# Performance work log

Hardware: AMD Instinct MI355X
Metric: run time of the kernel (lower is better)

The kernel has to match this reference:

```python
import jax, jax.numpy as jnp
import numpy as np

D_MODEL = 1024
N_HEADS = 16
D_K = D_MODEL // N_HEADS
NEG_INF = -1e30


def setup_inputs() -> dict:
    key = jax.random.key(0)
    ks = jax.random.split(key, 12)
    B, S = 4, 2048
    scale = 1.0 / np.sqrt(D_MODEL)
    inp = {
        "query": jax.random.normal(ks[0], (B, S, D_MODEL), jnp.float32),
        "key": jax.random.normal(ks[1], (B, S, D_MODEL), jnp.float32),
        "value": jax.random.normal(ks[2], (B, S, D_MODEL), jnp.float32),
        "mask": jax.random.randint(ks[3], (B, S, S), 0, 2, jnp.int32),
        "w_q": jax.random.normal(ks[4], (D_MODEL, D_MODEL), jnp.float32) * scale,
        "b_q": jnp.zeros((D_MODEL,), jnp.float32),
        "w_k": jax.random.normal(ks[5], (D_MODEL, D_MODEL), jnp.float32) * scale,
        "b_k": jnp.zeros((D_MODEL,), jnp.float32),
        "w_v": jax.random.normal(ks[6], (D_MODEL, D_MODEL), jnp.float32) * scale,
        "b_v": jnp.zeros((D_MODEL,), jnp.float32),
        "w_o": jax.random.normal(ks[7], (D_MODEL, D_MODEL), jnp.float32) * scale,
        "b_o": jnp.zeros((D_MODEL,), jnp.float32),
    }
    return inp


def reference(query, key, value, mask, w_q, b_q, w_k, b_k, w_v, b_v, w_o, b_o):
    B, Sq, _ = query.shape
    Sk = key.shape[1]
    # Linear projections (torch nn.Linear: x @ W.T + b), split into heads
    Q = (query @ w_q.T + b_q).reshape(B, Sq, N_HEADS, D_K).transpose(0, 2, 1, 3)
    K = (key @ w_k.T + b_k).reshape(B, Sk, N_HEADS, D_K).transpose(0, 2, 1, 3)
    V = (value @ w_v.T + b_v).reshape(B, Sk, N_HEADS, D_K).transpose(0, 2, 1, 3)
    # scores: (B, H, Sq, Sk)
    scores = jnp.einsum('bhqd,bhkd->bhqk', Q, K) / jnp.sqrt(jnp.float32(D_K))
    scores = jnp.where(mask[:, None, :, :] == 0, NEG_INF, scores)
    attn = jax.nn.softmax(scores, axis=-1)  # dropout p=0 -> identity (eval)
    context = jnp.einsum('bhqk,bhkd->bhqd', attn, V)
    context = context.transpose(0, 2, 1, 3).reshape(B, Sq, D_MODEL)
    return context @ w_o.T + b_o
```

## Files before the change

### kernel.cpp

```cpp
#include <hip/hip_runtime.h>
#include <hip/hip_bf16.h>
#include <stdint.h>

#define DM 1024
#define NHEADS 16
#define DK 64
#define BB 4
#define SS 2048

typedef unsigned short u16;
typedef __bf16 bf16x8 __attribute__((ext_vector_type(8)));
typedef __bf16 bf16x4 __attribute__((ext_vector_type(4)));
typedef float f32x4 __attribute__((ext_vector_type(4)));

#if __has_builtin(__builtin_amdgcn_exp2f)
#define EXP2(x) __builtin_amdgcn_exp2f(x)
#else
#define EXP2(x) exp2f(x)
#endif

static __device__ __forceinline__ u16 f2bf(float f) {
    union { float f; uint32_t u; } v; v.f = f;
    uint32_t r = v.u + 0x7fffu + ((v.u >> 16) & 1u);
    return (u16)(r >> 16);
}

static __device__ __forceinline__ f32x4 mfma16(bf16x8 a, bf16x8 b, f32x4 c) {
    return __builtin_amdgcn_mfma_f32_16x16x32_bf16(a, b, c, 0, 0, 0);
}

static __device__ __forceinline__ void gload16(const u16* g, u16* l) {
    __builtin_amdgcn_global_load_lds((const __attribute__((address_space(1))) void*)g,
                                     (__attribute__((address_space(3))) void*)l, 16, 0, 0);
}

__global__ void k_cvtw(const float* __restrict__ wq, const float* __restrict__ wk,
                       const float* __restrict__ wv, const float* __restrict__ wo,
                       u16* __restrict__ out) {
    int t = blockIdx.x * blockDim.x + threadIdx.x;
    int which = t >> 18;
    int off = (t & 0x3FFFF) << 2;
    const float* src = (which == 0) ? wq : (which == 1) ? wk : (which == 2) ? wv : wo;
    float4 v = *(const float4*)(src + off);
    ushort4 o;
    o.x = f2bf(v.x); o.y = f2bf(v.y); o.z = f2bf(v.z); o.w = f2bf(v.w);
    *(ushort4*)(out + ((size_t)which << 20) + off) = o;
}

__global__ void k_cvtx(const float* __restrict__ q, const float* __restrict__ k,
                       const float* __restrict__ v, u16* __restrict__ out) {
    int bid = blockIdx.x;
    int which = bid >> 12;
    const float* src = (which == 0) ? q : (which == 1) ? k : v;
    size_t base = (((size_t)(bid & 4095)) * 256 + threadIdx.x) * 8;
    float4 v0 = *(const float4*)(src + base);
    float4 v1 = *(const float4*)(src + base + 4);
    union { u16 s[8]; uint4 u; } p;
    p.s[0]=f2bf(v0.x); p.s[1]=f2bf(v0.y); p.s[2]=f2bf(v0.z); p.s[3]=f2bf(v0.w);
    p.s[4]=f2bf(v1.x); p.s[5]=f2bf(v1.y); p.s[6]=f2bf(v1.z); p.s[7]=f2bf(v1.w);
    *(uint4*)(out + ((size_t)which << 23) + base) = p.u;
}

__global__ void k_packmask(const int* __restrict__ mask, uint32_t* __restrict__ bits) {
    int gid = blockIdx.x * blockDim.x + threadIdx.x;
    int lane = gid & 63;
    int wv = gid >> 6;
    int nw = (gridDim.x * blockDim.x) >> 6;
    const long totalInts = (long)BB * SS * SS;
    for (long base = (long)wv * 64; base < totalInts; base += (long)nw * 64) {
        int m = mask[base + lane];
        unsigned long long bal = __ballot(m != 0);
        if (lane == 0)  bits[(base >> 5)]     = (uint32_t)bal;
        if (lane == 32) bits[(base >> 5) + 1] = (uint32_t)(bal >> 32);
    }
}

template<int MODE>
__global__ __launch_bounds__(256) void k_proj(const u16* __restrict__ X, const u16* __restrict__ W,
                                              const float* __restrict__ bias, void* __restrict__ Yv,
                                              float alpha) {
    __shared__ u16 Ab[128 * 32];
    __shared__ u16 Bb[128 * 32];
    const int tid = threadIdx.x;
    const int lane = tid & 63, wv = tid >> 6;
    const int wr = wv >> 1, wc = wv & 1;
    const int lrow = lane & 15, lgrp = lane >> 4;
    const int m0 = (blockIdx.x >> 3) * 128;
    const int n0 = (blockIdx.x & 7) * 128;
    const int trow = tid >> 2;
    const int tk = (tid & 3) * 8;

    f32x4 acc[4][4] = {};

    for (int kk = 0; kk < DM; kk += 32) {
#pragma unroll
        for (int i = 0; i < 2; ++i) {
            gload16(X + (size_t)(m0 + i * 64 + trow) * DM + kk + tk, &Ab[(i * 256 + tid) * 8]);
            gload16(W + (size_t)(n0 + i * 64 + trow) * DM + kk + tk, &Bb[(i * 256 + tid) * 8]);
        }
        __syncthreads();
        bf16x8 af[4], bfr[4];
#pragma unroll
        for (int i = 0; i < 4; ++i)
            af[i] = *(const bf16x8*)&Ab[(wr * 64 + i * 16 + lrow) * 32 + lgrp * 8];
#pragma unroll
        for (int j = 0; j < 4; ++j)
            bfr[j] = *(const bf16x8*)&Bb[(wc * 64 + j * 16 + lrow) * 32 + lgrp * 8];
#pragma unroll
        for (int i = 0; i < 4; ++i)
#pragma unroll
            for (int j = 0; j < 4; ++j)
                acc[i][j] = mfma16(af[i], bfr[j], acc[i][j]);
        __syncthreads();
    }

#pragma unroll
    for (int j = 0; j < 4; ++j) {
        int n = n0 + wc * 64 + j * 16 + lrow;
        float bv = bias[n];
        int h = n >> 6, d = n & 63;
#pragma unroll
        for (int i = 0; i < 4; ++i) {
            int mbase = m0 + wr * 64 + i * 16 + (lgrp << 2);
            if (MODE == 0) {
                u16* Y = (u16*)Yv;
#pragma unroll
                for (int r = 0; r < 4; ++r) {
                    int m = mbase + r;
                    int b = m >> 11, s = m & 2047;
                    Y[(((size_t)(b * NHEADS + h) * SS) + s) * DK + d] = f2bf((acc[i][j][r] + bv) * alpha);
                }
            } else if (MODE == 1) {
                int b = mbase >> 11, s = mbase & 2047;
                ushort4 o;
                o.x = f2bf(acc[i][j][0] + bv);
                o.y = f2bf(acc[i][j][1] + bv);
                o.z = f2bf(acc[i][j][2] + bv);
                o.w = f2bf(acc[i][j][3] + bv);
                *(ushort4*)&((u16*)Yv)[(((size_t)(b * NHEADS + h) * DK) + d) * SS + s] = o;
            } else {
                float* Y = (float*)Yv;
#pragma unroll
                for (int r = 0; r < 4; ++r)
                    Y[(size_t)(mbase + r) * DM + n] = acc[i][j][r] + bv;
            }
        }
    }
}

#define NT (SS / 64)
__global__ __launch_bounds__(256, 2) void k_attn(const u16* __restrict__ Q, const u16* __restrict__ K,
                                                 const u16* __restrict__ VT, const uint32_t* __restrict__ mbits,
                                                 u16* __restrict__ ctx) {
    __shared__ u16 Kt[2][64 * 64];
    __shared__ u16 Vt[2][64 * 64];
    __shared__ u16 Pl[4][2][16][72];
    const int tid = threadIdx.x;
    const int lane = tid & 63, w = tid >> 6;
    const int lrow = lane & 15, lgrp = lane >> 4;
    const int bid = blockIdx.x;
    const int x = bid & 7, rr_ = bid >> 3;
    const int h = (x & 3) + 4 * (rr_ & 3);
    const int qt = ((x >> 2) & 1) + 2 * ((rr_ >> 2) & 3);
    const int b = rr_ >> 4;
    const int bh = b * NHEADS + h;
    const int qbase = qt * 256 + w * 64;

    const u16* Qh = Q + (size_t)bh * SS * DK;
    const u16* Kh = K + (size_t)bh * SS * DK;
    const u16* Vh = VT + (size_t)bh * DK * SS;

    bf16x8 qf[4][2];
#pragma unroll
    for (int s = 0; s < 4; ++s) {
        const u16* p = Qh + (size_t)(qbase + 16 * s + lrow) * DK + lgrp * 8;
        qf[s][0] = *(const bf16x8*)(p);
        qf[s][1] = *(const bf16x8*)(p + 32);
    }

    const uint64_t* mrow[4];
#pragma unroll
    for (int s = 0; s < 4; ++s)
        mrow[s] = (const uint64_t*)mbits + ((size_t)(b * SS + qbase + 16 * s + lrow)) * (SS / 64);

    union { uint4 u; bf16x8 v; } onesu;
    onesu.u = make_uint4(0x3F803F80u, 0x3F803F80u, 0x3F803F80u, 0x3F803F80u);
    const bf16x8 ones = onesu.v;

    const int swzA = (lgrp * 8) ^ ((lrow & 7) * 8);
    const int swzB = (32 + lgrp * 8) ^ ((lrow & 7) * 8);

    f32x4 acc[4][4] = {};
    f32x4 asum[4] = {};

#pragma unroll
    for (int i = 0; i < 2; ++i) {
        int li = i * 256 + tid;
        int row = li >> 3;
        int src = ((li & 7) * 8) ^ ((row & 7) * 8);
        gload16(Kh + (size_t)(row)*DK + src, &Kt[0][li * 8]);
        gload16(Vh + (size_t)(row)*SS + src, &Vt[0][li * 8]);
    }
    __syncthreads();

    int cur = 0;
    for (int kt = 0; kt < NT; ++kt) {
        if (kt + 1 < NT) {
#pragma unroll
            for (int i = 0; i < 2; ++i) {
                int li = i * 256 + tid;
                int row = li >> 3;
                int src = ((li & 7) * 8) ^ ((row & 7) * 8);
                gload16(Kh + (size_t)((kt + 1) * 64 + row) * DK + src, &Kt[cur ^ 1][li * 8]);
                gload16(Vh + (size_t)(row)*SS + (kt + 1) * 64 + src, &Vt[cur ^ 1][li * 8]);
            }
        }
        uint64_t wm4[4];
#pragma unroll
        for (int s = 0; s < 4; ++s) wm4[s] = mrow[s][kt];

        const u16* Kc = Kt[cur];
        const u16* Vc = Vt[cur];
        bf16x8 pf[4][2];
#pragma unroll
        for (int sg = 0; sg < 2; ++sg) {
            f32x4 st[2][4] = {};
#pragma unroll
            for (int t = 0; t < 4; ++t) {
                bf16x8 ka = *(const bf16x8*)&Kc[(16 * t + lrow) * 64 + swzA];
                bf16x8 kb = *(const bf16x8*)&Kc[(16 * t + lrow) * 64 + swzB];
                st[0][t] = mfma16(ka, qf[2 * sg + 0][0], st[0][t]);
                st[0][t] = mfma16(kb, qf[2 * sg + 0][1], st[0][t]);
                st[1][t] = mfma16(ka, qf[2 * sg + 1][0], st[1][t]);
                st[1][t] = mfma16(kb, qf[2 * sg + 1][1], st[1][t]);
            }
#pragma unroll
            for (int s2 = 0; s2 < 2; ++s2) {
                const int s = 2 * sg + s2;
                const uint64_t wm = wm4[s];
#pragma unroll
                for (int t = 0; t < 4; ++t) {
                    uint32_t wt = (uint32_t)(wm >> (16 * t + 4 * lgrp));
                    bf16x4 pk;
#pragma unroll
                    for (int r = 0; r < 4; ++r) {
                        float p = EXP2(st[s2][t][r]);
                        p = ((wt >> r) & 1u) ? p : 0.0f;
                        pk[r] = (__bf16)p;
                    }
                    *(bf16x4*)&Pl[w][s2][lrow][16 * t + 4 * lgrp] = pk;
                }
            }
#pragma unroll
            for (int s2 = 0; s2 < 2; ++s2) {
                const int s = 2 * sg + s2;
                pf[s][0] = *(const bf16x8*)&Pl[w][s2][lrow][lgrp * 8];
                pf[s][1] = *(const bf16x8*)&Pl[w][s2][lrow][32 + lgrp * 8];
                asum[s] = mfma16(pf[s][0], ones, asum[s]);
                asum[s] = mfma16(pf[s][1], ones, asum[s]);
            }
        }
#pragma unroll
        for (int dt = 0; dt < 4; ++dt) {
            bf16x8 vf0 = *(const bf16x8*)&Vc[(16 * dt + lrow) * 64 + swzA];
            bf16x8 vf1 = *(const bf16x8*)&Vc[(16 * dt + lrow) * 64 + swzB];
#pragma unroll
            for (int s = 0; s < 4; ++s) {
                acc[s][dt] = mfma16(pf[s][0], vf0, acc[s][dt]);
                acc[s][dt] = mfma16(pf[s][1], vf1, acc[s][dt]);
            }
        }
        __syncthreads();
        cur ^= 1;
    }

#pragma unroll
    for (int s = 0; s < 4; ++s)
#pragma unroll
        for (int r = 0; r < 4; ++r) {
            float li = 1.0f / asum[s][r];
            int q = qbase + 16 * s + 4 * lgrp + r;
#pragma unroll
            for (int dt = 0; dt < 4; ++dt)
                ctx[((size_t)b * SS + q) * DM + h * 64 + dt * 16 + lrow] = f2bf(acc[s][dt][r] * li);
        }
}

extern "C" void kernel_launch(void* const* d_in, const int* in_sizes, int n_in,
                              void* d_out, int out_size, void* d_ws, size_t ws_size,
                              hipStream_t stream) {
    const float* query = (const float*)d_in[0];
    const float* key   = (const float*)d_in[1];
    const float* value = (const float*)d_in[2];
    const int*   mask  = (const int*)d_in[3];
    const float* w_q   = (const float*)d_in[4];
    const float* b_q   = (const float*)d_in[5];
    const float* w_k   = (const float*)d_in[6];
    const float* b_k   = (const float*)d_in[7];
    const float* w_v   = (const float*)d_in[8];
    const float* b_v   = (const float*)d_in[9];
    const float* w_o   = (const float*)d_in[10];
    const float* b_o   = (const float*)d_in[11];
    float* out = (float*)d_out;

    char* ws = (char*)d_ws;
    u16*      Wb = (u16*)(ws);
    uint32_t* mb = (uint32_t*)(ws + (8u  << 20));
    u16*      Xq = (u16*)(ws + (16u << 20));
    u16*      Xk = (u16*)(ws + (32u << 20));
    u16*      Xv = (u16*)(ws + (48u << 20));
    u16*      Qw = (u16*)(ws + (64u << 20));
    u16*      Kw = (u16*)(ws + (80u << 20));
    u16*      Vw = (u16*)(ws + (96u << 20));
    u16*      Cw = (u16*)(ws + (112u << 20));

    const float qscale = 0.125f * 1.4426950408889634f;

    k_cvtw<<<dim3(4096), dim3(256), 0, stream>>>(w_q, w_k, w_v, w_o, Wb);
    k_cvtx<<<dim3(12288), dim3(256), 0, stream>>>(query, key, value, Xq);
    k_packmask<<<dim3(2048), dim3(256), 0, stream>>>(mask, mb);
    k_proj<0><<<dim3(512), dim3(256), 0, stream>>>(Xq, Wb,              b_q, Qw, qscale);
    k_proj<0><<<dim3(512), dim3(256), 0, stream>>>(Xk, Wb + (1u << 20), b_k, Kw, 1.0f);
    k_proj<1><<<dim3(512), dim3(256), 0, stream>>>(Xv, Wb + (2u << 20), b_v, Vw, 1.0f);
    k_attn<<<dim3(512), dim3(256), 0, stream>>>(Qw, Kw, Vw, mb, Cw);
    k_proj<2><<<dim3(512), dim3(256), 0, stream>>>(Cw, Wb + (3u << 20), b_o, out, 1.0f);
}
```

Baseline: 287.9 us.

## Merge preprocessing kernels and widen attention blocks to 8 waves of 32 rows

```diff
diff --git a/kernel.cpp b/kernel.cpp
--- a/kernel.cpp
+++ b/kernel.cpp
@@ -34,44 +34,49 @@
                                      (__attribute__((address_space(3))) void*)l, 16, 0, 0);
 }
 
-__global__ void k_cvtw(const float* __restrict__ wq, const float* __restrict__ wk,
-                       const float* __restrict__ wv, const float* __restrict__ wo,
-                       u16* __restrict__ out) {
-    int t = blockIdx.x * blockDim.x + threadIdx.x;
-    int which = t >> 18;
-    int off = (t & 0x3FFFF) << 2;
-    const float* src = (which == 0) ? wq : (which == 1) ? wk : (which == 2) ? wv : wo;
-    float4 v = *(const float4*)(src + off);
-    ushort4 o;
-    o.x = f2bf(v.x); o.y = f2bf(v.y); o.z = f2bf(v.z); o.w = f2bf(v.w);
-    *(ushort4*)(out + ((size_t)which << 20) + off) = o;
-}
-
-__global__ void k_cvtx(const float* __restrict__ q, const float* __restrict__ k,
-                       const float* __restrict__ v, u16* __restrict__ out) {
-    int bid = blockIdx.x;
-    int which = bid >> 12;
-    const float* src = (which == 0) ? q : (which == 1) ? k : v;
-    size_t base = (((size_t)(bid & 4095)) * 256 + threadIdx.x) * 8;
-    float4 v0 = *(const float4*)(src + base);
-    float4 v1 = *(const float4*)(src + base + 4);
-    union { u16 s[8]; uint4 u; } p;
-    p.s[0]=f2bf(v0.x); p.s[1]=f2bf(v0.y); p.s[2]=f2bf(v0.z); p.s[3]=f2bf(v0.w);
-    p.s[4]=f2bf(v1.x); p.s[5]=f2bf(v1.y); p.s[6]=f2bf(v1.z); p.s[7]=f2bf(v1.w);
-    *(uint4*)(out + ((size_t)which << 23) + base) = p.u;
-}
-
-__global__ void k_packmask(const int* __restrict__ mask, uint32_t* __restrict__ bits) {
-    int gid = blockIdx.x * blockDim.x + threadIdx.x;
-    int lane = gid & 63;
-    int wv = gid >> 6;
-    int nw = (gridDim.x * blockDim.x) >> 6;
-    const long totalInts = (long)BB * SS * SS;
-    for (long base = (long)wv * 64; base < totalInts; base += (long)nw * 64) {
-        int m = mask[base + lane];
-        unsigned long long bal = __ballot(m != 0);
-        if (lane == 0)  bits[(base >> 5)]     = (uint32_t)bal;
-        if (lane == 32) bits[(base >> 5) + 1] = (uint32_t)(bal >> 32);
+#define PREP_W 4096
+#define PREP_X 12288
+#define PREP_M 2048
+__global__ __launch_bounds__(256) void k_prep(const float* __restrict__ wq, const float* __restrict__ wk,
+                                              const float* __restrict__ wv, const float* __restrict__ wo,
+                                              u16* __restrict__ wout,
+                                              const float* __restrict__ xq, const float* __restrict__ xk,
+                                              const float* __restrict__ xv, u16* __restrict__ xout,
+                                              const int* __restrict__ mask, uint32_t* __restrict__ bits) {
+    const int bid = blockIdx.x, tid = threadIdx.x;
+    if (bid < PREP_W) {
+        int t = bid * 256 + tid;
+        int which = t >> 18;
+        int off = (t & 0x3FFFF) << 2;
+        const float* src = (which == 0) ? wq : (which == 1) ? wk : (which == 2) ? wv : wo;
+        float4 v = *(const float4*)(src + off);
+        ushort4 o;
+        o.x = f2bf(v.x); o.y = f2bf(v.y); o.z = f2bf(v.z); o.w = f2bf(v.w);
+        *(ushort4*)(wout + ((size_t)which << 20) + off) = o;
+    } else if (bid < PREP_W + PREP_X) {
+        int lb = bid - PREP_W;
+        int which = lb >> 12;
+        const float* src = (which == 0) ? xq : (which == 1) ? xk : xv;
+        size_t base = (((size_t)(lb & 4095)) * 256 + tid) * 8;
+        float4 v0 = *(const float4*)(src + base);
+        float4 v1 = *(const float4*)(src + base + 4);
+        union { u16 s[8]; uint4 u; } p;
+        p.s[0]=f2bf(v0.x); p.s[1]=f2bf(v0.y); p.s[2]=f2bf(v0.z); p.s[3]=f2bf(v0.w);
+        p.s[4]=f2bf(v1.x); p.s[5]=f2bf(v1.y); p.s[6]=f2bf(v1.z); p.s[7]=f2bf(v1.w);
+        *(uint4*)(xout + ((size_t)which << 23) + base) = p.u;
+    } else {
+        int lb = bid - PREP_W - PREP_X;
+        int gid = lb * 256 + tid;
+        int lane = gid & 63;
+        int wv_ = gid >> 6;
+        const int nw = (PREP_M * 256) >> 6;
+        const long totalInts = (long)BB * SS * SS;
+        for (long base = (long)wv_ * 64; base < totalInts; base += (long)nw * 64) {
+            int m = mask[base + lane];
+            unsigned long long bal = __ballot(m != 0);
+            if (lane == 0)  bits[(base >> 5)]     = (uint32_t)bal;
+            if (lane == 32) bits[(base >> 5) + 1] = (uint32_t)(bal >> 32);
+        }
     }
 }
 
@@ -149,38 +154,36 @@
 }
 
 #define NT (SS / 64)
-__global__ __launch_bounds__(256, 2) void k_attn(const u16* __restrict__ Q, const u16* __restrict__ K,
+__global__ __launch_bounds__(512, 4) void k_attn(const u16* __restrict__ Q, const u16* __restrict__ K,
                                                  const u16* __restrict__ VT, const uint32_t* __restrict__ mbits,
                                                  u16* __restrict__ ctx) {
     __shared__ u16 Kt[2][64 * 64];
     __shared__ u16 Vt[2][64 * 64];
-    __shared__ u16 Pl[4][2][16][72];
+    __shared__ u16 Pl[8][2][16][72];
     const int tid = threadIdx.x;
     const int lane = tid & 63, w = tid >> 6;
     const int lrow = lane & 15, lgrp = lane >> 4;
     const int bid = blockIdx.x;
-    const int x = bid & 7, rr_ = bid >> 3;
-    const int h = (x & 3) + 4 * (rr_ & 3);
-    const int qt = ((x >> 2) & 1) + 2 * ((rr_ >> 2) & 3);
-    const int b = rr_ >> 4;
-    const int bh = b * NHEADS + h;
-    const int qbase = qt * 256 + w * 64;
+    const int bh = bid & 63;
+    const int qt = bid >> 6;
+    const int b = bh >> 4, h = bh & 15;
+    const int qbase = qt * 256 + w * 32;
 
     const u16* Qh = Q + (size_t)bh * SS * DK;
     const u16* Kh = K + (size_t)bh * SS * DK;
     const u16* Vh = VT + (size_t)bh * DK * SS;
 
-    bf16x8 qf[4][2];
-#pragma unroll
-    for (int s = 0; s < 4; ++s) {
+    bf16x8 qf[2][2];
+#pragma unroll
+    for (int s = 0; s < 2; ++s) {
         const u16* p = Qh + (size_t)(qbase + 16 * s + lrow) * DK + lgrp * 8;
         qf[s][0] = *(const bf16x8*)(p);
         qf[s][1] = *(const bf16x8*)(p + 32);
     }
 
-    const uint64_t* mrow[4];
-#pragma unroll
-    for (int s = 0; s < 4; ++s)
+    const uint64_t* mrow[2];
+#pragma unroll
+    for (int s = 0; s < 2; ++s)
         mrow[s] = (const uint64_t*)mbits + ((size_t)(b * SS + qbase + 16 * s + lrow)) * (SS / 64);
 
     union { uint4 u; bf16x8 v; } onesu;
@@ -190,82 +193,63 @@
     const int swzA = (lgrp * 8) ^ ((lrow & 7) * 8);
     const int swzB = (32 + lgrp * 8) ^ ((lrow & 7) * 8);
 
-    f32x4 acc[4][4] = {};
-    f32x4 asum[4] = {};
-
-#pragma unroll
-    for (int i = 0; i < 2; ++i) {
-        int li = i * 256 + tid;
-        int row = li >> 3;
-        int src = ((li & 7) * 8) ^ ((row & 7) * 8);
-        gload16(Kh + (size_t)(row)*DK + src, &Kt[0][li * 8]);
-        gload16(Vh + (size_t)(row)*SS + src, &Vt[0][li * 8]);
-    }
+    const int srow = tid >> 3;
+    const int ssrc = ((tid & 7) * 8) ^ ((srow & 7) * 8);
+
+    f32x4 acc[2][4] = {};
+    f32x4 asum[2] = {};
+
+    gload16(Kh + (size_t)srow * DK + ssrc, &Kt[0][tid * 8]);
+    gload16(Vh + (size_t)srow * SS + ssrc, &Vt[0][tid * 8]);
     __syncthreads();
 
     int cur = 0;
     for (int kt = 0; kt < NT; ++kt) {
         if (kt + 1 < NT) {
-#pragma unroll
-            for (int i = 0; i < 2; ++i) {
-                int li = i * 256 + tid;
-                int row = li >> 3;
-                int src = ((li & 7) * 8) ^ ((row & 7) * 8);
-                gload16(Kh + (size_t)((kt + 1) * 64 + row) * DK + src, &Kt[cur ^ 1][li * 8]);
-                gload16(Vh + (size_t)(row)*SS + (kt + 1) * 64 + src, &Vt[cur ^ 1][li * 8]);
-            }
-        }
-        uint64_t wm4[4];
-#pragma unroll
-        for (int s = 0; s < 4; ++s) wm4[s] = mrow[s][kt];
+            gload16(Kh + (size_t)((kt + 1) * 64 + srow) * DK + ssrc, &Kt[cur ^ 1][tid * 8]);
+            gload16(Vh + (size_t)srow * SS + (kt + 1) * 64 + ssrc, &Vt[cur ^ 1][tid * 8]);
+        }
+        uint64_t wm2[2];
+#pragma unroll
+        for (int s = 0; s < 2; ++s) wm2[s] = mrow[s][kt];
 
         const u16* Kc = Kt[cur];
         const u16* Vc = Vt[cur];
-        bf16x8 pf[4][2];
-#pragma unroll
-        for (int sg = 0; sg < 2; ++sg) {
-            f32x4 st[2][4] = {};
+        bf16x8 pf[2][2];
+#pragma unroll
+        for (int s = 0; s < 2; ++s) {
+            f32x4 st[4] = {};
 #pragma unroll
             for (int t = 0; t < 4; ++t) {
                 bf16x8 ka = *(const bf16x8*)&Kc[(16 * t + lrow) * 64 + swzA];
                 bf16x8 kb = *(const bf16x8*)&Kc[(16 * t + lrow) * 64 + swzB];
-                st[0][t] = mfma16(ka, qf[2 * sg + 0][0], st[0][t]);
-                st[0][t] = mfma16(kb, qf[2 * sg + 0][1], st[0][t]);
-                st[1][t] = mfma16(ka, qf[2 * sg + 1][0], st[1][t]);
-                st[1][t] = mfma16(kb, qf[2 * sg + 1][1], st[1][t]);
+                st[t] = mfma16(ka, qf[s][0], st[t]);
+                st[t] = mfma16(kb, qf[s][1], st[t]);
             }
-#pragma unroll
-            for (int s2 = 0; s2 < 2; ++s2) {
-                const int s = 2 * sg + s2;
-                const uint64_t wm = wm4[s];
-#pragma unroll
-                for (int t = 0; t < 4; ++t) {
-                    uint32_t wt = (uint32_t)(wm >> (16 * t + 4 * lgrp));
-                    bf16x4 pk;
-#pragma unroll
-                    for (int r = 0; r < 4; ++r) {
-                        float p = EXP2(st[s2][t][r]);
-                        p = ((wt >> r) & 1u) ? p : 0.0f;
-                        pk[r] = (__bf16)p;
-                    }
-                    *(bf16x4*)&Pl[w][s2][lrow][16 * t + 4 * lgrp] = pk;
+            const uint64_t wm = wm2[s];
+#pragma unroll
+            for (int t = 0; t < 4; ++t) {
+                uint32_t wt = (uint32_t)(wm >> (16 * t + 4 * lgrp));
+                bf16x4 pk;
+#pragma unroll
+                for (int r = 0; r < 4; ++r) {
+                    float p = EXP2(st[t][r]);
+                    p = ((wt >> r) & 1u) ? p : 0.0f;
+                    pk[r] = (__bf16)p;
                 }
+                *(bf16x4*)&Pl[w][s][lrow][16 * t + 4 * lgrp] = pk;
             }
-#pragma unroll
-            for (int s2 = 0; s2 < 2; ++s2) {
-                const int s = 2 * sg + s2;
-                pf[s][0] = *(const bf16x8*)&Pl[w][s2][lrow][lgrp * 8];
-                pf[s][1] = *(const bf16x8*)&Pl[w][s2][lrow][32 + lgrp * 8];
-                asum[s] = mfma16(pf[s][0], ones, asum[s]);
-                asum[s] = mfma16(pf[s][1], ones, asum[s]);
-            }
+            pf[s][0] = *(const bf16x8*)&Pl[w][s][lrow][lgrp * 8];
+            pf[s][1] = *(const bf16x8*)&Pl[w][s][lrow][32 + lgrp * 8];
+            asum[s] = mfma16(pf[s][0], ones, asum[s]);
+            asum[s] = mfma16(pf[s][1], ones, asum[s]);
         }
 #pragma unroll
         for (int dt = 0; dt < 4; ++dt) {
             bf16x8 vf0 = *(const bf16x8*)&Vc[(16 * dt + lrow) * 64 + swzA];
             bf16x8 vf1 = *(const bf16x8*)&Vc[(16 * dt + lrow) * 64 + swzB];
 #pragma unroll
-            for (int s = 0; s < 4; ++s) {
+            for (int s = 0; s < 2; ++s) {
                 acc[s][dt] = mfma16(pf[s][0], vf0, acc[s][dt]);
                 acc[s][dt] = mfma16(pf[s][1], vf1, acc[s][dt]);
             }
@@ -275,7 +259,7 @@
     }
 
 #pragma unroll
-    for (int s = 0; s < 4; ++s)
+    for (int s = 0; s < 2; ++s)
 #pragma unroll
         for (int r = 0; r < 4; ++r) {
             float li = 1.0f / asum[s][r];
@@ -316,12 +300,11 @@
 
     const float qscale = 0.125f * 1.4426950408889634f;
 
-    k_cvtw<<<dim3(4096), dim3(256), 0, stream>>>(w_q, w_k, w_v, w_o, Wb);
-    k_cvtx<<<dim3(12288), dim3(256), 0, stream>>>(query, key, value, Xq);
-    k_packmask<<<dim3(2048), dim3(256), 0, stream>>>(mask, mb);
+    k_prep<<<dim3(PREP_W + PREP_X + PREP_M), dim3(256), 0, stream>>>(
+        w_q, w_k, w_v, w_o, Wb, query, key, value, Xq, mask, mb);
     k_proj<0><<<dim3(512), dim3(256), 0, stream>>>(Xq, Wb,              b_q, Qw, qscale);
     k_proj<0><<<dim3(512), dim3(256), 0, stream>>>(Xk, Wb + (1u << 20), b_k, Kw, 1.0f);
     k_proj<1><<<dim3(512), dim3(256), 0, stream>>>(Xv, Wb + (2u << 20), b_v, Vw, 1.0f);
-    k_attn<<<dim3(512), dim3(256), 0, stream>>>(Qw, Kw, Vw, mb, Cw);
+    k_attn<<<dim3(512), dim3(512), 0, stream>>>(Qw, Kw, Vw, mb, Cw);
     k_proj<2><<<dim3(512), dim3(256), 0, stream>>>(Cw, Wb + (3u << 20), b_o, out, 1.0f);
 }
```

After: 278.7 us. -3.2%, faster.
